# Optimization experiments

Hardware: AMD Instinct MI355X
Metric: run time of the kernel (lower is better)

## Reference

```python
import jax, jax.numpy as jnp
import numpy as np


def _seg_mean(h_src, src, dst, n_dst):
    # gather neighbor features along edges, then segment-mean onto dst nodes
    msgs = h_src[src]                                  # [E, F]
    s = jax.ops.segment_sum(msgs, dst, num_segments=n_dst)
    deg = jax.ops.segment_sum(jnp.ones_like(dst, dtype=h_src.dtype), dst, num_segments=n_dst)
    return s / jnp.maximum(deg, 1.0)[:, None]          # zero-degree -> 0


def _sage_conv(h_src, h_dst, src, dst, n_dst, W, b):
    h_N = _seg_mean(h_src, src, dst, n_dst)            # [n_dst, F]
    h_total = jnp.concatenate([h_dst, h_N], axis=1)    # [n_dst, 2F]
    return h_total @ W + b


def setup_inputs() -> dict:
    key = jax.random.key(0)
    ks = jax.random.split(key, 10)
    n_src1, n_dst1, n_dst2 = 200000, 50000, 10000
    E1, E2 = 1000000, 200000
    in_f, h_f, n_cls = 256, 256, 64
    x = jax.random.normal(ks[0], (n_src1, in_f), dtype=jnp.float32)
    W1 = jax.random.normal(ks[1], (2 * in_f, h_f), dtype=jnp.float32) * (1.0 / np.sqrt(2 * in_f))
    b1 = jax.random.normal(ks[2], (h_f,), dtype=jnp.float32) * 0.01
    W2 = jax.random.normal(ks[3], (2 * h_f, n_cls), dtype=jnp.float32) * (1.0 / np.sqrt(2 * h_f))
    b2 = jax.random.normal(ks[4], (n_cls,), dtype=jnp.float32) * 0.01
    src1 = jax.random.randint(ks[5], (E1,), 0, n_src1, dtype=jnp.int32)
    dst1 = jax.random.randint(ks[6], (E1,), 0, n_dst1, dtype=jnp.int32)
    src2 = jax.random.randint(ks[7], (E2,), 0, n_dst1, dtype=jnp.int32)
    dst2 = jax.random.randint(ks[8], (E2,), 0, n_dst2, dtype=jnp.int32)
    return {"x": x, "W1": W1, "b1": b1, "W2": W2, "b2": b2,
            "src1": src1, "dst1": dst1, "src2": src2, "dst2": dst2,
            "n_dst1": n_dst1, "n_dst2": n_dst2}


def reference(x, W1, b1, W2, b2, src1, dst1, src2, dst2, n_dst1, n_dst2):
    h_dst = x[:n_dst1]
    h = _sage_conv(x, h_dst, src1, dst1, n_dst1, W1, b1)
    h = jax.nn.relu(h)
    h_dst2 = h[:n_dst2]
    out = _sage_conv(h, h_dst2, src2, dst2, n_dst2, W2, b2)
    return out
```

## Files before the change

### kernel.cpp

```cpp
#include <hip/hip_runtime.h>
#include <hip/hip_bf16.h>

#define N_DST1 50000
#define N_DST2 10000
#define FEAT   256

typedef unsigned int u32;
typedef __attribute__((ext_vector_type(4))) float f32x4;
typedef __attribute__((ext_vector_type(8))) short bf16x8;

__device__ __forceinline__ ushort f2bf(float f) {
    u32 u = __float_as_uint(f);
    u32 r = (u + 0x7FFFu + ((u >> 16) & 1u)) >> 16;
    return (ushort)r;
}
__device__ __forceinline__ float bf2f(ushort u) {
    return __uint_as_float(((u32)u) << 16);
}

__device__ __forceinline__ void gload_lds16(const void* g, void* l) {
    __builtin_amdgcn_global_load_lds(
        (const __attribute__((address_space(1))) u32*)g,
        (__attribute__((address_space(3))) u32*)l, 16, 0, 0);
}

__global__ __launch_bounds__(256) void prep_kernel(
    const float* __restrict__ x, ushort* __restrict__ xb, u32* __restrict__ xq,
    int n8, int n8h,
    const int* __restrict__ dst1, int E1, int* __restrict__ deg1,
    const int* __restrict__ dst2, int E2, int* __restrict__ deg2)
{
    int gid = blockIdx.x * blockDim.x + threadIdx.x;
    if (gid < n8) {
        const f32x4* p = (const f32x4*)x + (size_t)gid * 2;
        f32x4 a = __builtin_nontemporal_load(p);
        f32x4 b = __builtin_nontemporal_load(p + 1);
        if (xq) {
            u32 w0 = 0, w1 = 0;
            w0 = __builtin_amdgcn_cvt_pk_fp8_f32(a.x, a.y, w0, false);
            w0 = __builtin_amdgcn_cvt_pk_fp8_f32(a.z, a.w, w0, true);
            w1 = __builtin_amdgcn_cvt_pk_fp8_f32(b.x, b.y, w1, false);
            w1 = __builtin_amdgcn_cvt_pk_fp8_f32(b.z, b.w, w1, true);
            uint2 wv; wv.x = w0; wv.y = w1;
            *((uint2*)xq + gid) = wv;
        }
        if (gid < n8h) {
            ushort4 lo = make_ushort4(f2bf(a.x), f2bf(a.y), f2bf(a.z), f2bf(a.w));
            ushort4 hi = make_ushort4(f2bf(b.x), f2bf(b.y), f2bf(b.z), f2bf(b.w));
            ushort4* q = (ushort4*)xb + (size_t)gid * 2;
            q[0] = lo; q[1] = hi;
        }
        return;
    }
    int e = gid - n8;
    int e14 = E1 >> 2, e24 = E2 >> 2;
    if (e < e14) {
        int4 d4 = reinterpret_cast<const int4*>(dst1)[e];
        atomicAdd(&deg1[d4.x], 1); atomicAdd(&deg1[d4.y], 1);
        atomicAdd(&deg1[d4.z], 1); atomicAdd(&deg1[d4.w], 1);
        return;
    }
    e -= e14;
    if (e < e24) {
        int4 d4 = reinterpret_cast<const int4*>(dst2)[e];
        atomicAdd(&deg2[d4.x], 1); atomicAdd(&deg2[d4.y], 1);
        atomicAdd(&deg2[d4.z], 1); atomicAdd(&deg2[d4.w], 1);
        return;
    }
    e -= e24;
    int r1 = E1 & 3;
    if (e < r1) { atomicAdd(&deg1[dst1[E1 - r1 + e]], 1); return; }
    e -= r1;
    int r2 = E2 & 3;
    if (e < r2) { atomicAdd(&deg2[dst2[E2 - r2 + e]], 1); return; }
}

__global__ __launch_bounds__(1024) void scan_wt_kernel(
    const int* __restrict__ degA, int nA, int* __restrict__ offA, int* __restrict__ posA,
    const int* __restrict__ degB, int nB, int* __restrict__ offB, int* __restrict__ posB,
    const float* __restrict__ W1, ushort* __restrict__ W1T,
    const float* __restrict__ W2, ushort* __restrict__ W2T)
{
    if (blockIdx.x >= 2) {
        int k = blockIdx.x - 2;
        int t = threadIdx.x;
        if (t < 256) W1T[(size_t)t * 512 + k] = f2bf(W1[(size_t)k * 256 + t]);
        else if (t < 320) {
            int n = t - 256;
            W2T[(size_t)n * 512 + k] = f2bf(W2[(size_t)k * 64 + n]);
        }
        return;
    }
    const int* deg = (blockIdx.x == 0) ? degA : degB;
    int*       off = (blockIdx.x == 0) ? offA : offB;
    int*       pos = (blockIdx.x == 0) ? posA : posB;
    int n = (blockIdx.x == 0) ? nA : nB;
    int n4 = n >> 2;

    __shared__ int wsum[16];
    __shared__ int carry_s;
    int t = threadIdx.x;
    int lane = t & 63, wid = t >> 6;
    if (t == 0) carry_s = 0;
    __syncthreads();
    for (int base = 0; base < n4; base += 1024) {
        int i = base + t;
        int4 v = make_int4(0, 0, 0, 0);
        if (i < n4) v = reinterpret_cast<const int4*>(deg)[i];
        int tot = v.x + v.y + v.z + v.w;
        int s = tot;
        #pragma unroll
        for (int d = 1; d < 64; d <<= 1) {
            int u = __shfl_up(s, d, 64);
            if (lane >= d) s += u;
        }
        if (lane == 63) wsum[wid] = s;
        __syncthreads();
        if (wid == 0 && lane < 16) {
            int ws = wsum[lane];
            #pragma unroll
            for (int d = 1; d < 16; d <<= 1) {
                int u = __shfl_up(ws, d, 64);
                if (lane >= d) ws += u;
            }
            wsum[lane] = ws;
        }
        __syncthreads();
        int waveoff = (wid == 0) ? 0 : wsum[wid - 1];
        int carry = carry_s;
        int base0 = carry + waveoff + s - tot;
        if (i < n4) {
            int4 e;
            e.x = base0;
            e.y = base0 + v.x;
            e.z = base0 + v.x + v.y;
            e.w = base0 + v.x + v.y + v.z;
            reinterpret_cast<int4*>(off)[i] = e;
            reinterpret_cast<int4*>(pos)[i] = e;
        }
        __syncthreads();
        if (t == 0) carry_s = carry + wsum[15];
        __syncthreads();
    }
    if (t == 0) off[n] = carry_s;
}

__global__ void scatter_csr2_kernel(const int* __restrict__ src1, const int* __restrict__ dst1,
                                    int E1, int* __restrict__ pos1, int* __restrict__ csr1,
                                    const int* __restrict__ src2, const int* __restrict__ dst2,
                                    int E2, int* __restrict__ pos2, int* __restrict__ csr2) {
    int e = blockIdx.x * blockDim.x + threadIdx.x;
    int e14 = E1 >> 2, e24 = E2 >> 2;
    if (e < e14) {
        int4 s4 = reinterpret_cast<const int4*>(src1)[e];
        int4 d4 = reinterpret_cast<const int4*>(dst1)[e];
        csr1[atomicAdd(&pos1[d4.x], 1)] = s4.x;
        csr1[atomicAdd(&pos1[d4.y], 1)] = s4.y;
        csr1[atomicAdd(&pos1[d4.z], 1)] = s4.z;
        csr1[atomicAdd(&pos1[d4.w], 1)] = s4.w;
        return;
    }
    e -= e14;
    if (e < e24) {
        int4 s4 = reinterpret_cast<const int4*>(src2)[e];
        int4 d4 = reinterpret_cast<const int4*>(dst2)[e];
        csr2[atomicAdd(&pos2[d4.x], 1)] = s4.x;
        csr2[atomicAdd(&pos2[d4.y], 1)] = s4.y;
        csr2[atomicAdd(&pos2[d4.z], 1)] = s4.z;
        csr2[atomicAdd(&pos2[d4.w], 1)] = s4.w;
        return;
    }
    e -= e24;
    int r1 = E1 & 3;
    if (e < r1) {
        int i = E1 - r1 + e;
        csr1[atomicAdd(&pos1[dst1[i]], 1)] = src1[i];
        return;
    }
    e -= r1;
    int r2 = E2 & 3;
    if (e < r2) {
        int i = E2 - r2 + e;
        csr2[atomicAdd(&pos2[dst2[i]], 1)] = src2[i];
        return;
    }
}

__global__ __launch_bounds__(512) void seg_mean_fp8_kernel(
    const u32* __restrict__ Xq, const int* __restrict__ off,
    const int* __restrict__ csr, ushort* __restrict__ out, int ndst)
{
    int wid = threadIdx.x >> 6;
    int d = blockIdx.x * 8 + wid;
    if (d >= ndst) return;
    int l = threadIdx.x & 63;
    int sub = l >> 4;
    int lg = l & 15;
    int beg = off[d], end = off[d + 1];
    float acc[16];
    #pragma unroll
    for (int q = 0; q < 16; ++q) acc[q] = 0.f;
    for (int j = beg; j < end; j += 8) {
        int i0 = j + sub, i1 = j + 4 + sub;
        int r0 = csr[min(i0, end - 1)];
        int r1 = csr[min(i1, end - 1)];
        uint4 v0 = *reinterpret_cast<const uint4*>(Xq + (size_t)r0 * 64 + lg * 4);
        uint4 v1 = *reinterpret_cast<const uint4*>(Xq + (size_t)r1 * 64 + lg * 4);
        float m0 = (i0 < end) ? 1.f : 0.f;
        float m1 = (i1 < end) ? 1.f : 0.f;
        u32 w0[4] = {v0.x, v0.y, v0.z, v0.w};
        u32 w1[4] = {v1.x, v1.y, v1.z, v1.w};
        #pragma unroll
        for (int w = 0; w < 4; ++w) {
            auto a01 = __builtin_amdgcn_cvt_pk_f32_fp8(w0[w], false);
            auto a23 = __builtin_amdgcn_cvt_pk_f32_fp8(w0[w], true);
            auto b01 = __builtin_amdgcn_cvt_pk_f32_fp8(w1[w], false);
            auto b23 = __builtin_amdgcn_cvt_pk_f32_fp8(w1[w], true);
            acc[w * 4 + 0] += m0 * a01[0] + m1 * b01[0];
            acc[w * 4 + 1] += m0 * a01[1] + m1 * b01[1];
            acc[w * 4 + 2] += m0 * a23[0] + m1 * b23[0];
            acc[w * 4 + 3] += m0 * a23[1] + m1 * b23[1];
        }
    }
    #pragma unroll
    for (int q = 0; q < 16; ++q) {
        acc[q] += __shfl_xor(acc[q], 16);
        acc[q] += __shfl_xor(acc[q], 32);
    }
    if (l < 16) {
        float sc = 1.0f / (float)max(end - beg, 1);
        bf16x8 o0, o1;
        #pragma unroll
        for (int q = 0; q < 8; ++q) {
            o0[q] = (short)f2bf(acc[q] * sc);
            o1[q] = (short)f2bf(acc[8 + q] * sc);
        }
        ushort* base = out + (size_t)d * FEAT + lg * 16;
        *reinterpret_cast<bf16x8*>(base) = o0;
        *reinterpret_cast<bf16x8*>(base + 8) = o1;
    }
}

__global__ __launch_bounds__(512) void seg_mean_bf16_kernel(
    const ushort* __restrict__ X, const int* __restrict__ off,
    const int* __restrict__ csr, ushort* __restrict__ out, int ndst)
{
    int wid = threadIdx.x >> 6;
    int d = blockIdx.x * 8 + wid;
    if (d >= ndst) return;
    int l = threadIdx.x & 63;
    int half = l >> 5;
    int f8 = (l & 31) * 8;
    int beg = off[d], end = off[d + 1];
    float acc[8] = {0.f, 0.f, 0.f, 0.f, 0.f, 0.f, 0.f, 0.f};
    for (int j = beg; j < end; j += 8) {
        #pragma unroll
        for (int p = 0; p < 4; ++p) {
            int idx = j + p * 2 + half;
            int r = csr[min(idx, end - 1)];
            bf16x8 v = *reinterpret_cast<const bf16x8*>(&X[(size_t)r * FEAT + f8]);
            float m = (idx < end) ? 1.f : 0.f;
            #pragma unroll
            for (int q = 0; q < 8; ++q) acc[q] += m * bf2f((ushort)v[q]);
        }
    }
    #pragma unroll
    for (int q = 0; q < 8; ++q) acc[q] += __shfl_xor(acc[q], 32);
    if (l < 32) {
        float sc = 1.0f / (float)max(end - beg, 1);
        bf16x8 ov;
        #pragma unroll
        for (int q = 0; q < 8; ++q) ov[q] = (short)f2bf(acc[q] * sc);
        *reinterpret_cast<bf16x8*>(&out[(size_t)d * FEAT + f8]) = ov;
    }
}

__global__ void seg_mean_f32_kernel(const float* __restrict__ X, const int* __restrict__ off,
                                    const int* __restrict__ csr, ushort* __restrict__ out) {
    int d = blockIdx.x;
    int t = threadIdx.x;
    int beg = off[d], end = off[d + 1];
    float a0 = 0.f, a1 = 0.f, a2 = 0.f, a3 = 0.f;
    for (int j = beg; j < end; ++j) {
        int s = csr[j];
        float4 v = *reinterpret_cast<const float4*>(&X[(size_t)s * FEAT + t * 4]);
        a0 += v.x; a1 += v.y; a2 += v.z; a3 += v.w;
    }
    float sc = 1.0f / (float)max(end - beg, 1);
    ushort4 o = make_ushort4(f2bf(a0 * sc), f2bf(a1 * sc), f2bf(a2 * sc), f2bf(a3 * sc));
    *reinterpret_cast<ushort4*>(&out[(size_t)d * FEAT + t * 4]) = o;
}

template<int BM, int BN, int WGM, int WGN, bool RELU, bool OBF16>
__global__ __launch_bounds__(WGM * WGN * 64)
void gemm_mfma_kernel(const ushort* __restrict__ A0, const ushort* __restrict__ A1,
                      const ushort* __restrict__ BT, const float* __restrict__ bias,
                      ushort* __restrict__ Cb, float* __restrict__ Cf,
                      int M, int Nfull) {
    constexpr int NWAVE = WGM * WGN;
    constexpr int WM = BM / WGM;
    constexpr int WN = BN / WGN;
    constexpr int MF = WM / 16;
    constexpr int NF = WN / 16;
    constexpr int ACH = BM / 16;
    constexpr int BCH = BN / 16;

    __shared__ ushort Al[2][BM][32];
    __shared__ ushort Bl[2][BN][32];

    const int t = threadIdx.x;
    const int lane = t & 63;
    const int wid = t >> 6;
    const int wm = wid / WGN, wn = wid % WGN;
    const int lr = lane & 15, grp = lane >> 4;
    const int rowBase = blockIdx.y * BM;
    const int colBase = blockIdx.x * BN;

    f32x4 acc[MF][NF];
    #pragma unroll
    for (int m = 0; m < MF; ++m)
        #pragma unroll
        for (int n = 0; n < NF; ++n)
            acc[m][n] = (f32x4){0.f, 0.f, 0.f, 0.f};

    auto stage = [&](int buf, int kt) {
        const ushort* Asrc = (kt < 8) ? A0 : A1;
        const int kcol = (kt * 32) & 255;
        #pragma unroll
        for (int ch = wid; ch < ACH; ch += NWAVE) {
            int r = ch * 16 + (lane >> 2);
            int rg = min(rowBase + r, M - 1);
            int c = lane & 3;
            int ksw = (c ^ (r & 3)) * 8;
            gload_lds16(&Asrc[(size_t)rg * 256 + kcol + ksw], &Al[buf][ch * 16][0]);
        }
        #pragma unroll
        for (int ch = wid; ch < BCH; ch += NWAVE) {
            int r = ch * 16 + (lane >> 2);
            int c = lane & 3;
            int ksw = (c ^ (r & 3)) * 8;
            gload_lds16(&BT[(size_t)(colBase + r) * 512 + kt * 32 + ksw], &Bl[buf][ch * 16][0]);
        }
    };

    stage(0, 0);
    __syncthreads();

    int buf = 0;
    for (int kt = 0; kt < 16; ++kt) {
        if (kt + 1 < 16) stage(buf ^ 1, kt + 1);
        bf16x8 af[MF], bfr[NF];
        #pragma unroll
        for (int m = 0; m < MF; ++m) {
            int r = wm * WM + m * 16 + lr;
            af[m] = *reinterpret_cast<const bf16x8*>(
                (const char*)&Al[buf][0][0] + r * 64 + ((grp ^ (r & 3)) << 4));
        }
        #pragma unroll
        for (int n = 0; n < NF; ++n) {
            int r = wn * WN + n * 16 + lr;
            bfr[n] = *reinterpret_cast<const bf16x8*>(
                (const char*)&Bl[buf][0][0] + r * 64 + ((grp ^ (r & 3)) << 4));
        }
        #pragma unroll
        for (int m = 0; m < MF; ++m)
            #pragma unroll
            for (int n = 0; n < NF; ++n)
                acc[m][n] = __builtin_amdgcn_mfma_f32_16x16x32_bf16(af[m], bfr[n], acc[m][n], 0, 0, 0);
        __syncthreads();
        buf ^= 1;
    }

    #pragma unroll
    for (int m = 0; m < MF; ++m) {
        #pragma unroll
        for (int q = 0; q < 4; ++q) {
            int rowg = rowBase + wm * WM + m * 16 + grp * 4 + q;
            if (rowg >= M) continue;
            #pragma unroll
            for (int n = 0; n < NF; ++n) {
                int colg = colBase + wn * WN + n * 16 + lr;
                float v = acc[m][n][q] + bias[colg];
                if (RELU) v = fmaxf(v, 0.f);
                if (OBF16) Cb[(size_t)rowg * Nfull + colg] = f2bf(v);
                else       Cf[(size_t)rowg * Nfull + colg] = v;
            }
        }
    }
}

extern "C" void kernel_launch(void* const* d_in, const int* in_sizes, int n_in,
                              void* d_out, int out_size, void* d_ws, size_t ws_size,
                              hipStream_t stream) {
    const float* x  = (const float*)d_in[0];
    const float* W1 = (const float*)d_in[1];
    const float* b1 = (const float*)d_in[2];
    const float* W2 = (const float*)d_in[3];
    const float* b2 = (const float*)d_in[4];
    const int* src1 = (const int*)d_in[5];
    const int* dst1 = (const int*)d_in[6];
    const int* src2 = (const int*)d_in[7];
    const int* dst2 = (const int*)d_in[8];
    const int E1 = in_sizes[5];
    const int E2 = in_sizes[7];
    const int N_SRC1 = in_sizes[0] / FEAT;
    float* out = (float*)d_out;

    char* ws = (char*)d_ws;
    size_t o = 0;
    auto carve = [&](size_t bytes) { char* p = ws + o; o = (o + bytes + 255) & ~(size_t)255; return p; };
    int*    degs = (int*)   carve((size_t)(N_DST1 + N_DST2) * 4);
    int*    deg1 = degs;
    int*    deg2 = degs + N_DST1;
    int*    off1 = (int*)   carve((size_t)(N_DST1 + 1) * 4);
    int*    pos1 = (int*)   carve((size_t)N_DST1 * 4);
    int*    csr1 = (int*)   carve((size_t)E1 * 4);
    ushort* hN1b = (ushort*)carve((size_t)N_DST1 * FEAT * 2);
    ushort* hb   = (ushort*)carve((size_t)N_DST1 * FEAT * 2);
    int*    off2 = (int*)   carve((size_t)(N_DST2 + 1) * 4);
    int*    pos2 = (int*)   carve((size_t)N_DST2 * 4);
    int*    csr2 = (int*)   carve((size_t)E2 * 4);
    ushort* hN2b = (ushort*)carve((size_t)N_DST2 * FEAT * 2);
    ushort* W1T  = (ushort*)carve((size_t)256 * 512 * 2);
    ushort* W2T  = (ushort*)carve((size_t)64 * 512 * 2);
    ushort* xb = (ushort*)carve((size_t)N_DST1 * FEAT * 2);
    size_t q_bytes = (size_t)N_SRC1 * FEAT;
    bool fp8path = (o + q_bytes) <= ws_size;
    u32* xq = fp8path ? (u32*)carve(q_bytes) : nullptr;

    (void)hipMemsetAsync(degs, 0, (size_t)(N_DST1 + N_DST2) * 4, stream);
    {
        int n8  = (fp8path ? N_SRC1 : N_DST1) * FEAT / 8;
        int n8h = N_DST1 * FEAT / 8;
        int tot = n8 + (E1 >> 2) + (E2 >> 2) + (E1 & 3) + (E2 & 3);
        prep_kernel<<<(tot + 255) / 256, 256, 0, stream>>>(
            x, xb, xq, n8, n8h, dst1, E1, deg1, dst2, E2, deg2);
    }
    scan_wt_kernel<<<514, 1024, 0, stream>>>(deg1, N_DST1, off1, pos1,
                                             deg2, N_DST2, off2, pos2,
                                             W1, W1T, W2, W2T);
    {
        int tot = (E1 >> 2) + (E2 >> 2) + (E1 & 3) + (E2 & 3);
        scatter_csr2_kernel<<<(tot + 255) / 256, 256, 0, stream>>>(
            src1, dst1, E1, pos1, csr1, src2, dst2, E2, pos2, csr2);
    }

    if (fp8path)
        seg_mean_fp8_kernel<<<(N_DST1 + 7) / 8, 512, 0, stream>>>(xq, off1, csr1, hN1b, N_DST1);
    else
        seg_mean_f32_kernel<<<N_DST1, 64, 0, stream>>>(x, off1, csr1, hN1b);
    gemm_mfma_kernel<128, 256, 2, 4, true, true><<<dim3(1, (N_DST1 + 127) / 128), 512, 0, stream>>>(
        xb, hN1b, W1T, b1, hb, nullptr, N_DST1, 256);

    seg_mean_bf16_kernel<<<(N_DST2 + 7) / 8, 512, 0, stream>>>(hb, off2, csr2, hN2b, N_DST2);
    gemm_mfma_kernel<64, 64, 2, 2, false, false><<<dim3(1, (N_DST2 + 63) / 64), 256, 0, stream>>>(
        hb, hN2b, W2T, b2, nullptr, out, N_DST2, 64);
}
```

Baseline: 303.2 us.

## Add chunked thread-per-dst FP8 layer-1 gather and FP8 copy of hidden for layer 2

```diff
diff --git a/kernel.cpp b/kernel.cpp
--- a/kernel.cpp
+++ b/kernel.cpp
@@ -6,6 +6,7 @@
 #define FEAT   256
 
 typedef unsigned int u32;
+typedef unsigned char u8;
 typedef __attribute__((ext_vector_type(4))) float f32x4;
 typedef __attribute__((ext_vector_type(8))) short bf16x8;
 
@@ -16,6 +17,10 @@
 }
 __device__ __forceinline__ float bf2f(ushort u) {
     return __uint_as_float(((u32)u) << 16);
+}
+__device__ __forceinline__ u8 f2fp8(float f) {
+    u32 pk = __builtin_amdgcn_cvt_pk_fp8_f32(f, f, 0, false);
+    return (u8)(pk & 0xFF);
 }
 
 __device__ __forceinline__ void gload_lds16(const void* g, void* l) {
@@ -186,6 +191,65 @@
     }
 }
 
+__global__ __launch_bounds__(256) void seg_mean_fp8_chunked_kernel(
+    const u8* __restrict__ Xq, const int* __restrict__ off,
+    const int* __restrict__ csr, ushort* __restrict__ out, int ndst)
+{
+    int c = blockIdx.x & 7;
+    int d = (blockIdx.x >> 3) * 256 + threadIdx.x;
+    if (d >= ndst) return;
+    int beg = off[d], end = off[d + 1];
+    float acc[32];
+    #pragma unroll
+    for (int q = 0; q < 32; ++q) acc[q] = 0.f;
+    const u8* base = Xq + (size_t)c * 32;
+    int j = beg;
+    for (; j + 2 <= end; j += 2) {
+        int r0 = csr[j], r1 = csr[j + 1];
+        uint4 a0 = *reinterpret_cast<const uint4*>(base + (size_t)r0 * 256);
+        uint4 a1 = *reinterpret_cast<const uint4*>(base + (size_t)r0 * 256 + 16);
+        uint4 b0 = *reinterpret_cast<const uint4*>(base + (size_t)r1 * 256);
+        uint4 b1 = *reinterpret_cast<const uint4*>(base + (size_t)r1 * 256 + 16);
+        u32 wa[8] = {a0.x, a0.y, a0.z, a0.w, a1.x, a1.y, a1.z, a1.w};
+        u32 wb[8] = {b0.x, b0.y, b0.z, b0.w, b1.x, b1.y, b1.z, b1.w};
+        #pragma unroll
+        for (int q = 0; q < 8; ++q) {
+            auto alo = __builtin_amdgcn_cvt_pk_f32_fp8(wa[q], false);
+            auto ahi = __builtin_amdgcn_cvt_pk_f32_fp8(wa[q], true);
+            auto blo = __builtin_amdgcn_cvt_pk_f32_fp8(wb[q], false);
+            auto bhi = __builtin_amdgcn_cvt_pk_f32_fp8(wb[q], true);
+            acc[q * 4 + 0] += alo[0] + blo[0];
+            acc[q * 4 + 1] += alo[1] + blo[1];
+            acc[q * 4 + 2] += ahi[0] + bhi[0];
+            acc[q * 4 + 3] += ahi[1] + bhi[1];
+        }
+    }
+    if (j < end) {
+        int r0 = csr[j];
+        uint4 a0 = *reinterpret_cast<const uint4*>(base + (size_t)r0 * 256);
+        uint4 a1 = *reinterpret_cast<const uint4*>(base + (size_t)r0 * 256 + 16);
+        u32 wa[8] = {a0.x, a0.y, a0.z, a0.w, a1.x, a1.y, a1.z, a1.w};
+        #pragma unroll
+        for (int q = 0; q < 8; ++q) {
+            auto alo = __builtin_amdgcn_cvt_pk_f32_fp8(wa[q], false);
+            auto ahi = __builtin_amdgcn_cvt_pk_f32_fp8(wa[q], true);
+            acc[q * 4 + 0] += alo[0];
+            acc[q * 4 + 1] += alo[1];
+            acc[q * 4 + 2] += ahi[0];
+            acc[q * 4 + 3] += ahi[1];
+        }
+    }
+    float sc = 1.0f / (float)max(end - beg, 1);
+    ushort* ob = out + (size_t)d * FEAT + c * 32;
+    #pragma unroll
+    for (int g = 0; g < 4; ++g) {
+        bf16x8 ov;
+        #pragma unroll
+        for (int q = 0; q < 8; ++q) ov[q] = (short)f2bf(acc[g * 8 + q] * sc);
+        *reinterpret_cast<bf16x8*>(ob + g * 8) = ov;
+    }
+}
+
 __global__ __launch_bounds__(512) void seg_mean_fp8_kernel(
     const u32* __restrict__ Xq, const int* __restrict__ off,
     const int* __restrict__ csr, ushort* __restrict__ out, int ndst)
@@ -291,11 +355,11 @@
     *reinterpret_cast<ushort4*>(&out[(size_t)d * FEAT + t * 4]) = o;
 }
 
-template<int BM, int BN, int WGM, int WGN, bool RELU, bool OBF16>
+template<int BM, int BN, int WGM, int WGN, bool RELU, bool OBF16, bool WQ8>
 __global__ __launch_bounds__(WGM * WGN * 64)
 void gemm_mfma_kernel(const ushort* __restrict__ A0, const ushort* __restrict__ A1,
                       const ushort* __restrict__ BT, const float* __restrict__ bias,
-                      ushort* __restrict__ Cb, float* __restrict__ Cf,
+                      ushort* __restrict__ Cb, float* __restrict__ Cf, u8* __restrict__ Cq,
                       int M, int Nfull) {
     constexpr int NWAVE = WGM * WGN;
     constexpr int WM = BM / WGM;
@@ -384,6 +448,7 @@
                 if (RELU) v = fmaxf(v, 0.f);
                 if (OBF16) Cb[(size_t)rowg * Nfull + colg] = f2bf(v);
                 else       Cf[(size_t)rowg * Nfull + colg] = v;
+                if (WQ8)   Cq[(size_t)rowg * Nfull + colg] = f2fp8(v);
             }
         }
     }
@@ -417,6 +482,7 @@
     int*    csr1 = (int*)   carve((size_t)E1 * 4);
     ushort* hN1b = (ushort*)carve((size_t)N_DST1 * FEAT * 2);
     ushort* hb   = (ushort*)carve((size_t)N_DST1 * FEAT * 2);
+    u8*     hq   = (u8*)    carve((size_t)N_DST1 * FEAT);
     int*    off2 = (int*)   carve((size_t)(N_DST2 + 1) * 4);
     int*    pos2 = (int*)   carve((size_t)N_DST2 * 4);
     int*    csr2 = (int*)   carve((size_t)E2 * 4);
@@ -445,14 +511,23 @@
             src1, dst1, E1, pos1, csr1, src2, dst2, E2, pos2, csr2);
     }
 
-    if (fp8path)
-        seg_mean_fp8_kernel<<<(N_DST1 + 7) / 8, 512, 0, stream>>>(xq, off1, csr1, hN1b, N_DST1);
-    else
+    if (fp8path) {
+        int nblk = 8 * ((N_DST1 + 255) / 256);
+        seg_mean_fp8_chunked_kernel<<<nblk, 256, 0, stream>>>(
+            (const u8*)xq, off1, csr1, hN1b, N_DST1);
+        gemm_mfma_kernel<128, 256, 2, 4, true, true, true><<<dim3(1, (N_DST1 + 127) / 128), 512, 0, stream>>>(
+            xb, hN1b, W1T, b1, hb, nullptr, hq, N_DST1, 256);
+
+        seg_mean_fp8_kernel<<<(N_DST2 + 7) / 8, 512, 0, stream>>>(
+            (const u32*)hq, off2, csr2, hN2b, N_DST2);
+        gemm_mfma_kernel<64, 64, 2, 2, false, false, false><<<dim3(1, (N_DST2 + 63) / 64), 256, 0, stream>>>(
+            hb, hN2b, W2T, b2, nullptr, out, nullptr, N_DST2, 64);
+    } else {
         seg_mean_f32_kernel<<<N_DST1, 64, 0, stream>>>(x, off1, csr1, hN1b);
-    gemm_mfma_kernel<128, 256, 2, 4, true, true><<<dim3(1, (N_DST1 + 127) / 128), 512, 0, stream>>>(
-        xb, hN1b, W1T, b1, hb, nullptr, N_DST1, 256);
-
-    seg_mean_bf16_kernel<<<(N_DST2 + 7) / 8, 512, 0, stream>>>(hb, off2, csr2, hN2b, N_DST2);
-    gemm_mfma_kernel<64, 64, 2, 2, false, false><<<dim3(1, (N_DST2 + 63) / 64), 256, 0, stream>>>(
-        hb, hN2b, W2T, b2, nullptr, out, N_DST2, 64);
-}
+        gemm_mfma_kernel<128, 256, 2, 4, true, true, false><<<dim3(1, (N_DST1 + 127) / 128), 512, 0, stream>>>(
+            xb, hN1b, W1T, b1, hb, nullptr, nullptr, N_DST1, 256);
+        seg_mean_bf16_kernel<<<(N_DST2 + 7) / 8, 512, 0, stream>>>(hb, off2, csr2, hN2b, N_DST2);
+        gemm_mfma_kernel<64, 64, 2, 2, false, false, false><<<dim3(1, (N_DST2 + 63) / 64), 256, 0, stream>>>(
+            hb, hN2b, W2T, b2, nullptr, out, nullptr, N_DST2, 64);
+    }
+}
```

New measurement: 434.1 us. +43.2%, slower.
